# Performance work log

Hardware: AMD Instinct MI355X
Metric: run time of the kernel (lower is better)

## Reference

```python
import jax, jax.numpy as jnp
import numpy as np

B, T, D, H = 4, 2048, 1024, 16
HD = D // H  # 64


def setup_inputs() -> dict:
    key = jax.random.key(0)
    ks = jax.random.split(key, 5)
    return {
        "x": jax.random.normal(ks[0], (B, T, D), dtype=jnp.float32),
        "W_qkv": jax.random.normal(ks[1], (D, 3 * D), dtype=jnp.float32) * 0.02,
        "b_qkv": jax.random.normal(ks[2], (3 * D,), dtype=jnp.float32) * 0.02,
        "W_out": jax.random.normal(ks[3], (D, D), dtype=jnp.float32) * 0.02,
        "b_out": jax.random.normal(ks[4], (D,), dtype=jnp.float32) * 0.02,
        "mask": 1,
    }


def reference(x, W_qkv, b_qkv, W_out, b_out, mask):
    # fused QKV projection: (B,T,3D)
    qkv = x @ W_qkv + b_qkv
    # torch layout: view (B,T,H,3*hd) then chunk last dim into q,k,v
    qkv = qkv.reshape(B, T, H, 3, HD)
    q = qkv[..., 0, :].transpose(0, 2, 1, 3)  # (B,H,T,hd)
    k = qkv[..., 1, :].transpose(0, 2, 1, 3)
    v = qkv[..., 2, :].transpose(0, 2, 1, 3)
    scores = jnp.einsum('bhqd,bhkd->bhqk', q, k) / jnp.sqrt(jnp.float32(HD))
    if mask:
        causal = jnp.triu(jnp.ones((T, T), dtype=bool), k=1)
        scores = jnp.where(causal[None, None], jnp.float32(-jnp.inf), scores)
    attn = jax.nn.softmax(scores, axis=-1)
    out = jnp.einsum('bhqk,bhkd->bhqd', attn, v)  # (B,H,T,hd)
    out = out.transpose(0, 2, 1, 3).reshape(B, T, D)
    return out @ W_out + b_out
```

## Files before the change

### kernel.cpp

```cpp
#include <hip/hip_runtime.h>

typedef unsigned short u16;
typedef __bf16 bf16x8 __attribute__((ext_vector_type(8)));
typedef float f32x4 __attribute__((ext_vector_type(4)));
typedef float f32x16 __attribute__((ext_vector_type(16)));

#define DEV __device__ __forceinline__

constexpr int Bb = 4, Tt = 2048, Dd = 1024, Hh = 16, HDd = 64;
constexpr int MM = Bb * Tt;
constexpr float QSCALE = 0.125f * 1.4426950408889634f;

DEV u16 f2bf(float f) {
  unsigned u = __float_as_uint(f);
  u += 0x7fffu + ((u >> 16) & 1u);
  return (u16)(u >> 16);
}

DEV unsigned cvtpk(float a, float b) {
  unsigned r;
  asm("v_cvt_pk_bf16_f32 %0, %1, %2" : "=v"(r) : "v"(a), "v"(b));
  return r;
}

DEV void pswap(unsigned& a, unsigned& b) {
  asm("v_permlane32_swap_b32 %0, %1" : "+v"(a), "+v"(b));
}

DEV void gload_lds16(const u16* g, u16* l) {
  __builtin_amdgcn_global_load_lds(
      (const __attribute__((address_space(1))) void*)g,
      (__attribute__((address_space(3))) void*)l, 16, 0, 0);
}

__global__ __launch_bounds__(256) void cast_x_kernel(const float* __restrict__ in,
                                                     u16* __restrict__ out, int n8) {
  int i = blockIdx.x * 256 + threadIdx.x;
  if (i >= n8) return;
  const float4* p = (const float4*)in + (size_t)i * 2;
  float4 v0 = p[0], v1 = p[1];
  union { u16 u[8]; uint4 v; } t;
  t.u[0] = f2bf(v0.x); t.u[1] = f2bf(v0.y); t.u[2] = f2bf(v0.z); t.u[3] = f2bf(v0.w);
  t.u[4] = f2bf(v1.x); t.u[5] = f2bf(v1.y); t.u[6] = f2bf(v1.z); t.u[7] = f2bf(v1.w);
  ((uint4*)out)[i] = t.v;
}

__global__ __launch_bounds__(256) void wcast_t_kernel(const float* __restrict__ in,
                                                      u16* __restrict__ out, int K, int N) {
  __shared__ float tile[32][33];
  int n0 = blockIdx.x * 32, k0 = blockIdx.y * 32;
  int tx = threadIdx.x & 31, ty = threadIdx.x >> 5;
  #pragma unroll
  for (int yy = ty; yy < 32; yy += 8)
    tile[yy][tx] = in[(size_t)(k0 + yy) * N + n0 + tx];
  __syncthreads();
  #pragma unroll
  for (int yy = ty; yy < 32; yy += 8)
    out[(size_t)(n0 + yy) * K + k0 + tx] = f2bf(tile[tx][yy]);
}

DEV void stageA128(const u16* __restrict__ src, int row0, int k0, int ld, u16* lds) {
  int t = threadIdx.x;
  int r = t >> 2, slot = t & 3;
  int c = (slot ^ ((r >> 1) & 3)) << 3;
  gload_lds16(src + (size_t)(row0 + r) * ld + k0 + c, lds + (size_t)(t & ~63) * 8);
}
DEV void stageB256(const u16* __restrict__ src, int row0, int k0, int ld, u16* lds) {
  int t = threadIdx.x;
  #pragma unroll
  for (int j = 0; j < 2; ++j) {
    int e = j * 512 + t;
    int r = e >> 2, slot = e & 3;
    int c = (slot ^ ((r >> 1) & 3)) << 3;
    gload_lds16(src + (size_t)(row0 + r) * ld + k0 + c,
                lds + (size_t)(j * 512 + (t & ~63)) * 8);
  }
}

__global__ __launch_bounds__(512, 4) void gemm_qkv_kernel(
    const u16* __restrict__ A, const u16* __restrict__ Bt,
    const float* __restrict__ bias,
    u16* __restrict__ Qb, u16* __restrict__ Kb, u16* __restrict__ Vtb,
    int M, int N, int Kd) {
  __shared__ __align__(16) u16 SH[36864];
  int nx = N >> 8;
  int bid = blockIdx.y * nx + blockIdx.x;
  int nwg = (M >> 7) * nx;
  int swz = (bid & 7) * (nwg >> 3) + (bid >> 3);
  int m0 = (swz / nx) * 128, n0 = (swz % nx) * 256;

  int tid = threadIdx.x, l = tid & 63, w = tid >> 6;
  int lo = l & 15, g = l >> 4;
  int wm = (w >> 2) * 64, wn = (w & 3) * 64;
  f32x4 acc[4][4] = {};
  int nk = Kd >> 5;
  stageA128(A, m0, 0, Kd, SH);
  stageB256(Bt, n0, 0, Kd, SH + 12288);
  stageA128(A, m0, 32, Kd, SH + 4096);
  stageB256(Bt, n0, 32, Kd, SH + 12288 + 8192);
  asm volatile("s_waitcnt vmcnt(3)" ::: "memory");
  __builtin_amdgcn_s_barrier();
  for (int kt = 0; kt < nk; ++kt) {
    if (kt + 2 < nk) {
      int bi = (kt + 2) % 3;
      stageA128(A, m0, (kt + 2) * 32, Kd, SH + bi * 4096);
      stageB256(Bt, n0, (kt + 2) * 32, Kd, SH + 12288 + bi * 8192);
    }
    const u16* Ac = SH + (kt % 3) * 4096;
    const u16* Bc = SH + 12288 + (kt % 3) * 8192;
    bf16x8 a[4], b[4];
    #pragma unroll
    for (int i = 0; i < 4; ++i) {
      int row = wm + i * 16 + lo;
      a[i] = *(const bf16x8*)&Ac[row * 32 + ((g ^ ((row >> 1) & 3)) << 3)];
    }
    #pragma unroll
    for (int j = 0; j < 4; ++j) {
      int row = wn + j * 16 + lo;
      b[j] = *(const bf16x8*)&Bc[row * 32 + ((g ^ ((row >> 1) & 3)) << 3)];
    }
    __builtin_amdgcn_s_setprio(1);
    #pragma unroll
    for (int i = 0; i < 4; ++i)
      #pragma unroll
      for (int j = 0; j < 4; ++j)
        acc[i][j] = __builtin_amdgcn_mfma_f32_16x16x32_bf16(a[i], b[j], acc[i][j], 0, 0, 0);
    __builtin_amdgcn_s_setprio(0);
    if (kt + 2 < nk) {
      asm volatile("s_waitcnt vmcnt(3)" ::: "memory");
    } else {
      asm volatile("s_waitcnt vmcnt(0)" ::: "memory");
    }
    __builtin_amdgcn_s_barrier();
  }
  #pragma unroll
  for (int round = 0; round < 2; ++round) {
    if ((w >> 2) == round) {
      u16* ep = SH + (w & 3) * 4096;
      int nblk = n0 + wn;
      int hh = nblk / 192, which = (nblk % 192) >> 6;
      int mblk = m0 + wm;
      int b_ = mblk >> 11, t0 = mblk & (Tt - 1);
      if (which == 2) {
        #pragma unroll
        for (int j = 0; j < 4; ++j) {
          float bv = bias[nblk + j * 16 + lo];
          int rowp = j * 16 + lo;
          #pragma unroll
          for (int i = 0; i < 4; ++i) {
            int slotp = i * 2 + (g >> 1);
            #pragma unroll
            for (int r = 0; r < 4; ++r) {
              ep[rowp * 64 + ((slotp ^ (rowp & 7)) << 3) + (g & 1) * 4 + r] =
                  f2bf(acc[i][j][r] + bv);
            }
          }
        }
        asm volatile("s_waitcnt lgkmcnt(0)" ::: "memory");
        u16* dst = Vtb + (size_t)(b_ * Hh + hh) * HDd * Tt + t0;
        #pragma unroll
        for (int s = 0; s < 8; ++s) {
          int row = s * 8 + (l >> 3);
          int phys = ((l & 7) ^ (row & 7)) << 3;
          uint4 v = *(const uint4*)&ep[row * 64 + phys];
          *(uint4*)(dst + (size_t)row * Tt + (l & 7) * 8) = v;
        }
      } else {
        float qs = (which == 0) ? QSCALE : 1.0f;
        #pragma unroll
        for (int j = 0; j < 4; ++j) {
          float bv = bias[nblk + j * 16 + lo];
          int slot = j * 2 + (lo >> 3);
          #pragma unroll
          for (int i = 0; i < 4; ++i) {
            #pragma unroll
            for (int r = 0; r < 4; ++r) {
              int lrow = i * 16 + g * 4 + r;
              ep[lrow * 64 + ((slot ^ (lrow & 7)) << 3) + (lo & 7)] =
                  f2bf((acc[i][j][r] + bv) * qs);
            }
          }
        }
        asm volatile("s_waitcnt lgkmcnt(0)" ::: "memory");
        u16* dst = (which == 0) ? Qb : Kb;
        dst += ((size_t)(b_ * Hh + hh) * Tt + t0) * HDd;
        #pragma unroll
        for (int s = 0; s < 8; ++s) {
          int row = s * 8 + (l >> 3);
          int phys = ((l & 7) ^ (row & 7)) << 3;
          uint4 v = *(const uint4*)&ep[row * 64 + phys];
          *(uint4*)(dst + row * 64 + (l & 7) * 8) = v;
        }
      }
    }
    __syncthreads();
  }
}

__global__ __launch_bounds__(512, 4) void gemm_out256_kernel(
    const u16* __restrict__ A, const u16* __restrict__ Bt,
    const float* __restrict__ bias, float* __restrict__ Cf,
    int M, int N, int Kd) {
  __shared__ __align__(16) u16 SH[36864];
  int nx = N >> 8;
  int bid = blockIdx.y * nx + blockIdx.x;
  int nwg = (M >> 7) * nx;
  int swz = (bid & 7) * (nwg >> 3) + (bid >> 3);
  int m0 = (swz / nx) * 128, n0 = (swz % nx) * 256;

  int tid = threadIdx.x, l = tid & 63, w = tid >> 6;
  int lo = l & 15, g = l >> 4;
  int wm = (w >> 2) * 64, wn = (w & 3) * 64;
  f32x4 acc[4][4] = {};
  int nk = Kd >> 5;
  stageA128(A, m0, 0, Kd, SH);
  stageB256(Bt, n0, 0, Kd, SH + 12288);
  stageA128(A, m0, 32, Kd, SH + 4096);
  stageB256(Bt, n0, 32, Kd, SH + 12288 + 8192);
  asm volatile("s_waitcnt vmcnt(3)" ::: "memory");
  __builtin_amdgcn_s_barrier();
  for (int kt = 0; kt < nk; ++kt) {
    if (kt + 2 < nk) {
      int bi = (kt + 2) % 3;
      stageA128(A, m0, (kt + 2) * 32, Kd, SH + bi * 4096);
      stageB256(Bt, n0, (kt + 2) * 32, Kd, SH + 12288 + bi * 8192);
    }
    const u16* Ac = SH + (kt % 3) * 4096;
    const u16* Bc = SH + 12288 + (kt % 3) * 8192;
    bf16x8 a[4], b[4];
    #pragma unroll
    for (int i = 0; i < 4; ++i) {
      int row = wm + i * 16 + lo;
      a[i] = *(const bf16x8*)&Ac[row * 32 + ((g ^ ((row >> 1) & 3)) << 3)];
    }
    #pragma unroll
    for (int j = 0; j < 4; ++j) {
      int row = wn + j * 16 + lo;
      b[j] = *(const bf16x8*)&Bc[row * 32 + ((g ^ ((row >> 1) & 3)) << 3)];
    }
    __builtin_amdgcn_s_setprio(1);
    #pragma unroll
    for (int i = 0; i < 4; ++i)
      #pragma unroll
      for (int j = 0; j < 4; ++j)
        acc[i][j] = __builtin_amdgcn_mfma_f32_16x16x32_bf16(a[i], b[j], acc[i][j], 0, 0, 0);
    __builtin_amdgcn_s_setprio(0);
    if (kt + 2 < nk) {
      asm volatile("s_waitcnt vmcnt(3)" ::: "memory");
    } else {
      asm volatile("s_waitcnt vmcnt(0)" ::: "memory");
    }
    __builtin_amdgcn_s_barrier();
  }
  #pragma unroll
  for (int j = 0; j < 4; ++j) {
    int n = n0 + wn + j * 16 + lo;
    float bv = bias[n];
    #pragma unroll
    for (int i = 0; i < 4; ++i) {
      #pragma unroll
      for (int r = 0; r < 4; ++r) {
        int m = m0 + wm + i * 16 + g * 4 + r;
        Cf[(size_t)m * N + n] = acc[i][j][r] + bv;
      }
    }
  }
}

DEV void stage512(const u16* __restrict__ g, size_t rstride, u16* lds) {
  int t = threadIdx.x;
  int r = t >> 3, pp = t & 7;
  int lg = pp ^ (r & 7);
  gload_lds16(g + (size_t)r * rstride + lg * 8, lds + (size_t)(t & ~63) * 8);
}

DEV void build_pfrags(const f32x16& s, bf16x8& f0, bf16x8& f1) {
  unsigned w0 = cvtpk(s[0], s[1]),  w1 = cvtpk(s[2], s[3]);
  unsigned w2 = cvtpk(s[4], s[5]),  w3 = cvtpk(s[6], s[7]);
  unsigned w4 = cvtpk(s[8], s[9]),  w5 = cvtpk(s[10], s[11]);
  unsigned w6 = cvtpk(s[12], s[13]), w7 = cvtpk(s[14], s[15]);
  pswap(w0, w2);
  pswap(w1, w3);
  pswap(w4, w6);
  pswap(w5, w7);
  union { unsigned u[4]; bf16x8 v; } t0, t1;
  t0.u[0] = w0; t0.u[1] = w1; t0.u[2] = w2; t0.u[3] = w3;
  t1.u[0] = w4; t1.u[1] = w5; t1.u[2] = w6; t1.u[3] = w7;
  f0 = t0.v; f1 = t1.v;
}

DEV void write_o(u16* __restrict__ O, size_t rowbase, const f32x16& o0,
                 const f32x16& o1, float L, int hf) {
  float inv = 1.0f / L;
  #pragma unroll
  for (int m = 0; m < 4; ++m) {
    uint2 v0, v1;
    v0.x = cvtpk(o0[4 * m] * inv,     o0[4 * m + 1] * inv);
    v0.y = cvtpk(o0[4 * m + 2] * inv, o0[4 * m + 3] * inv);
    *(uint2*)(O + rowbase + m * 8 + hf * 4) = v0;
    v1.x = cvtpk(o1[4 * m] * inv,     o1[4 * m + 1] * inv);
    v1.y = cvtpk(o1[4 * m + 2] * inv, o1[4 * m + 3] * inv);
    *(uint2*)(O + rowbase + 32 + m * 8 + hf * 4) = v1;
  }
}

__global__ __launch_bounds__(512) void attn_kernel(const u16* __restrict__ Q,
                                                   const u16* __restrict__ K,
                                                   const u16* __restrict__ Vt,
                                                   u16* __restrict__ O) {
  __shared__ __align__(16) u16 Ks[4][4096];
  __shared__ __align__(16) u16 Vs[4][4096];
  __shared__ float MLs[8][64][2];
  __shared__ float OSs[4][64][4];
  int p = blockIdx.y & 7;
  int bh = ((int)blockIdx.y >> 3) * 8 + (int)blockIdx.x;
  int b_ = bh >> 4, h = bh & 15;
  const u16* Qp = Q + (size_t)bh * Tt * HDd;
  const u16* Kp = K + (size_t)bh * Tt * HDd;
  const u16* Vp = Vt + (size_t)bh * HDd * Tt;
  int tid = threadIdx.x, w = tid >> 6, l = tid & 63;
  int wq = w & 3, grp = w >> 2;
  int lq = l & 31, hf = l >> 5;
  int JA = 15 - p, JB = p;
  int ntA = 2 * JA + 2;
  constexpr int ntT = 34;

  int q0 = 128 * JA + 32 * wq;
  int qrow = q0 + lq;
  int swz = lq & 7;

  bf16x8 aq[4];
  #pragma unroll
  for (int s = 0; s < 4; ++s)
    aq[s] = *(const bf16x8*)(Qp + (size_t)qrow * HDd + s * 16 + hf * 8);

  f32x16 o0 = {}, o1 = {};
  float M = -1e30f, L = 0.f;

  stage512(Kp, HDd, Ks[0]);
  stage512(Vp, Tt, Vs[0]);
  stage512(Kp + (size_t)64 * HDd, HDd, Ks[1]);
  stage512(Vp + 64, Tt, Vs[1]);
  asm volatile("s_waitcnt vmcnt(0)" ::: "memory");
  __builtin_amdgcn_s_barrier();

  int jB = ntA >> 1;
  for (int j = 0; j < ntT / 2; ++j) {
    int t2 = 2 * j + 2;
    if (t2 < ntT) {
      int kt2 = (t2 < ntA ? t2 : t2 - ntA) * 64;
      stage512(Kp + (size_t)kt2 * HDd, HDd, Ks[t2 & 3]);
      stage512(Vp + kt2, Tt, Vs[t2 & 3]);
      int t3 = t2 + 1;
      int kt3 = (t3 < ntA ? t3 : t3 - ntA) * 64;
      stage512(Kp + (size_t)kt3 * HDd, HDd, Ks[t3 & 3]);
      stage512(Vp + kt3, Tt, Vs[t3 & 3]);
    }
    if (j == jB) {
      MLs[w][l][0] = M; MLs[w][l][1] = L;
      asm volatile("s_waitcnt lgkmcnt(0)" ::: "memory");
      __builtin_amdgcn_s_barrier();
      float Mb = MLs[w ^ 4][l][0], Lb = MLs[w ^ 4][l][1];
      float Mstar = fmaxf(M, Mb);
      float ss = __builtin_amdgcn_exp2f(M - Mstar);
      float sb = __builtin_amdgcn_exp2f(Mb - Mstar);
      float Lm = L * ss + Lb * sb;
      #pragma unroll
      for (int r = 0; r < 16; ++r) { o0[r] *= ss; o1[r] *= ss; }
      #pragma unroll
      for (int c = 0; c < 8; ++c) {
        if (w >= 4) {
          #pragma unroll
          for (int k = 0; k < 4; ++k)
            OSs[wq][l][k] = (c < 4) ? o0[c * 4 + k] : o1[(c - 4) * 4 + k];
        }
        asm volatile("s_waitcnt lgkmcnt(0)" ::: "memory");
        __builtin_amdgcn_s_barrier();
        if (w < 4) {
          #pragma unroll
          for (int k = 0; k < 4; ++k) {
            float v = OSs[wq][l][k];
            if (c < 4) o0[c * 4 + k] += v; else o1[(c - 4) * 4 + k] += v;
          }
        }
        asm volatile("s_waitcnt lgkmcnt(0)" ::: "memory");
        __builtin_amdgcn_s_barrier();
      }
      if (w < 4) {
        size_t rbA = ((size_t)b_ * Tt + qrow) * Dd + h * HDd;
        write_o(O, rbA, o0, o1, Lm, hf);
      }
      #pragma unroll
      for (int r = 0; r < 16; ++r) { o0[r] = 0.f; o1[r] = 0.f; }
      M = -1e30f; L = 0.f;
      q0 = 128 * JB + 32 * wq;
      qrow = q0 + lq;
      #pragma unroll
      for (int s = 0; s < 4; ++s)
        aq[s] = *(const bf16x8*)(Qp + (size_t)qrow * HDd + s * 16 + hf * 8);
    }
    int myt = 2 * j + grp;
    int kt = (myt < ntA ? myt : myt - ntA) * 64;
    const u16* Kc = Ks[myt & 3];
    const u16* Vc = Vs[myt & 3];
    if (kt < q0 + 32) {
      f32x16 s0 = {}, s1 = {};
      __builtin_amdgcn_s_setprio(1);
      #pragma unroll
      for (int ds = 0; ds < 4; ++ds) {
        int slot = 2 * ds + hf;
        bf16x8 k0 = *(const bf16x8*)&Kc[lq * 64 + ((slot ^ swz) << 3)];
        bf16x8 k1 = *(const bf16x8*)&Kc[(32 + lq) * 64 + ((slot ^ swz) << 3)];
        s0 = __builtin_amdgcn_mfma_f32_32x32x16_bf16(k0, aq[ds], s0, 0, 0, 0);
        s1 = __builtin_amdgcn_mfma_f32_32x32x16_bf16(k1, aq[ds], s1, 0, 0, 0);
      }
      __builtin_amdgcn_s_setprio(0);
      if (kt + 63 > q0) {
        #pragma unroll
        for (int r = 0; r < 16; ++r) {
          int kg = kt + (r & 3) + 8 * (r >> 2) + 4 * hf;
          if (kg > qrow)      s0[r] = -INFINITY;
          if (kg + 32 > qrow) s1[r] = -INFINITY;
        }
      }
      float mx_[16];
      #pragma unroll
      for (int r = 0; r < 16; ++r) mx_[r] = fmaxf(s0[r], s1[r]);
      #pragma unroll
      for (int st = 8; st >= 1; st >>= 1)
        #pragma unroll
        for (int r = 0; r < 16; ++r) if (r < st) mx_[r] = fmaxf(mx_[r], mx_[r + st]);
      float mx = fmaxf(mx_[0], __shfl_xor(mx_[0], 32));
      float sc = 1.f;
      if (!__all(mx <= M + 8.f)) {
        float Mn = fmaxf(M, mx);
        sc = __builtin_amdgcn_exp2f(M - Mn);
        M = Mn;
        #pragma unroll
        for (int r = 0; r < 16; ++r) { o0[r] *= sc; o1[r] *= sc; }
      }
      #pragma unroll
      for (int r = 0; r < 16; ++r) {
        s0[r] = __builtin_amdgcn_exp2f(s0[r] - M);
        s1[r] = __builtin_amdgcn_exp2f(s1[r] - M);
      }
      float ls_[16];
      #pragma unroll
      for (int r = 0; r < 16; ++r) ls_[r] = s0[r] + s1[r];
      #pragma unroll
      for (int st = 8; st >= 1; st >>= 1)
        #pragma unroll
        for (int r = 0; r < 16; ++r) if (r < st) ls_[r] += ls_[r + st];
      float ls = ls_[0] + __shfl_xor(ls_[0], 32);
      L = L * sc + ls;
      bf16x8 pf0, pf1, pf2, pf3;
      build_pfrags(s0, pf0, pf1);
      build_pfrags(s1, pf2, pf3);
      __builtin_amdgcn_s_setprio(1);
      #pragma unroll
      for (int ks = 0; ks < 4; ++ks) {
        int slot = 2 * ks + hf;
        bf16x8 v0 = *(const bf16x8*)&Vc[lq * 64 + ((slot ^ swz) << 3)];
        bf16x8 v1 = *(const bf16x8*)&Vc[(32 + lq) * 64 + ((slot ^ swz) << 3)];
        bf16x8 pf = (ks == 0) ? pf0 : (ks == 1) ? pf1 : (ks == 2) ? pf2 : pf3;
        o0 = __builtin_amdgcn_mfma_f32_32x32x16_bf16(v0, pf, o0, 0, 0, 0);
        o1 = __builtin_amdgcn_mfma_f32_32x32x16_bf16(v1, pf, o1, 0, 0, 0);
      }
      __builtin_amdgcn_s_setprio(0);
    }
    asm volatile("s_waitcnt vmcnt(0)" ::: "memory");
    __builtin_amdgcn_s_barrier();
  }

  MLs[w][l][0] = M; MLs[w][l][1] = L;
  asm volatile("s_waitcnt lgkmcnt(0)" ::: "memory");
  __builtin_amdgcn_s_barrier();
  float Mb = MLs[w ^ 4][l][0], Lb = MLs[w ^ 4][l][1];
  float Mstar = fmaxf(M, Mb);
  float ss = __builtin_amdgcn_exp2f(M - Mstar);
  float sb = __builtin_amdgcn_exp2f(Mb - Mstar);
  float Lm = L * ss + Lb * sb;
  #pragma unroll
  for (int r = 0; r < 16; ++r) { o0[r] *= ss; o1[r] *= ss; }
  #pragma unroll
  for (int c = 0; c < 8; ++c) {
    if (w >= 4) {
      #pragma unroll
      for (int k = 0; k < 4; ++k)
        OSs[wq][l][k] = (c < 4) ? o0[c * 4 + k] : o1[(c - 4) * 4 + k];
    }
    asm volatile("s_waitcnt lgkmcnt(0)" ::: "memory");
    __builtin_amdgcn_s_barrier();
    if (w < 4) {
      #pragma unroll
      for (int k = 0; k < 4; ++k) {
        float v = OSs[wq][l][k];
        if (c < 4) o0[c * 4 + k] += v; else o1[(c - 4) * 4 + k] += v;
      }
    }
    asm volatile("s_waitcnt lgkmcnt(0)" ::: "memory");
    __builtin_amdgcn_s_barrier();
  }
  if (w < 4) {
    size_t rbB = ((size_t)b_ * Tt + qrow) * Dd + h * HDd;
    write_o(O, rbB, o0, o1, Lm, hf);
  }
}

extern "C" void kernel_launch(void* const* d_in, const int* in_sizes, int n_in,
                              void* d_out, int out_size, void* d_ws, size_t ws_size,
                              hipStream_t stream) {
  const float* x    = (const float*)d_in[0];
  const float* Wqkv = (const float*)d_in[1];
  const float* bqkv = (const float*)d_in[2];
  const float* Wout = (const float*)d_in[3];
  const float* bout = (const float*)d_in[4];
  float* out = (float*)d_out;
  char* ws = (char*)d_ws;

  u16* xb    = (u16*)(ws + 0);
  u16* Ob    = (u16*)(ws + 0);
  u16* Wqkvt = (u16*)(ws + 16777216);
  u16* Woutt = (u16*)(ws + 23068672);
  u16* Qb    = (u16*)(ws + 25165824);
  u16* Kb    = (u16*)(ws + 41943040);
  u16* Vtb   = (u16*)(ws + 58720256);

  cast_x_kernel<<<4096, 256, 0, stream>>>(x, xb, (MM * Dd) / 8);
  wcast_t_kernel<<<dim3(96, 32), 256, 0, stream>>>(Wqkv, Wqkvt, Dd, 3 * Dd);
  wcast_t_kernel<<<dim3(32, 32), 256, 0, stream>>>(Wout, Woutt, Dd, Dd);
  gemm_qkv_kernel<<<dim3(12, 64), 512, 0, stream>>>(
      xb, Wqkvt, bqkv, Qb, Kb, Vtb, MM, 3 * Dd, Dd);
  attn_kernel<<<dim3(8, 64), 512, 0, stream>>>(Qb, Kb, Vtb, Ob);
  gemm_out256_kernel<<<dim3(4, 64), 512, 0, stream>>>(
      Ob, Woutt, bout, out, MM, Dd, Dd);
}
```

Baseline: 174.6 us.

## Split attention KV loop across four wave groups with 1024-thread blocks

Doubles the attention block to 16 waves, so four wave groups each take a different KV tile per iteration instead of two. The KV ring grows to 8 LDS slots and four tiles are staged per step. Partial softmax states are combined with a two-level merge (xor 8, then xor 4). The aim is more parallelism per query tile and half as many loop iterations. In exchange it pads the A-phase tile count to a multiple of four, which may add masked or wasted tiles, and adds LDS pressure, more barrier rounds in the merge, and launch_bounds(1024,1) register limits.

```diff
diff --git a/kernel.cpp b/kernel.cpp
--- a/kernel.cpp
+++ b/kernel.cpp
@@ -267,13 +267,6 @@
   }
 }
 
-DEV void stage512(const u16* __restrict__ g, size_t rstride, u16* lds) {
-  int t = threadIdx.x;
-  int r = t >> 3, pp = t & 7;
-  int lg = pp ^ (r & 7);
-  gload_lds16(g + (size_t)r * rstride + lg * 8, lds + (size_t)(t & ~63) * 8);
-}
-
 DEV void build_pfrags(const f32x16& s, bf16x8& f0, bf16x8& f1) {
   unsigned w0 = cvtpk(s[0], s[1]),  w1 = cvtpk(s[2], s[3]);
   unsigned w2 = cvtpk(s[4], s[5]),  w3 = cvtpk(s[6], s[7]);
@@ -304,14 +297,14 @@
   }
 }
 
-__global__ __launch_bounds__(512) void attn_kernel(const u16* __restrict__ Q,
-                                                   const u16* __restrict__ K,
-                                                   const u16* __restrict__ Vt,
-                                                   u16* __restrict__ O) {
-  __shared__ __align__(16) u16 Ks[4][4096];
-  __shared__ __align__(16) u16 Vs[4][4096];
-  __shared__ float MLs[8][64][2];
-  __shared__ float OSs[4][64][4];
+__global__ __launch_bounds__(1024, 1) void attn_kernel(const u16* __restrict__ Q,
+                                                       const u16* __restrict__ K,
+                                                       const u16* __restrict__ Vt,
+                                                       u16* __restrict__ O) {
+  __shared__ __align__(16) u16 Ks[8][4096];
+  __shared__ __align__(16) u16 Vs[8][4096];
+  __shared__ float MLs[16][64][2];
+  __shared__ float OSs[8][64][4];
   int p = blockIdx.y & 7;
   int bh = ((int)blockIdx.y >> 3) * 8 + (int)blockIdx.x;
   int b_ = bh >> 4, h = bh & 15;
@@ -323,7 +316,8 @@
   int lq = l & 31, hf = l >> 5;
   int JA = 15 - p, JB = p;
   int ntA = 2 * JA + 2;
-  constexpr int ntT = 34;
+  int ntAp = (ntA + 3) & ~3;
+  int jA = ntAp >> 2;
 
   int q0 = 128 * JA + 32 * wq;
   int qrow = q0 + lq;
@@ -337,58 +331,71 @@
   f32x16 o0 = {}, o1 = {};
   float M = -1e30f, L = 0.f;
 
-  stage512(Kp, HDd, Ks[0]);
-  stage512(Vp, Tt, Vs[0]);
-  stage512(Kp + (size_t)64 * HDd, HDd, Ks[1]);
-  stage512(Vp + 64, Tt, Vs[1]);
+  auto slot_kt = [&](int s) { return (s < ntAp ? s : s - ntAp) * 64; };
+  auto stage2K = [&](int s) {
+    int s2 = s + (tid >> 9), c = tid & 511;
+    int kt2 = slot_kt(s2);
+    int r = c >> 3, pp = c & 7;
+    int lg = pp ^ (r & 7);
+    gload_lds16(Kp + (size_t)(kt2 + r) * HDd + lg * 8,
+                Ks[s2 & 7] + (size_t)(c & ~63) * 8);
+  };
+  auto stage2V = [&](int s) {
+    int s2 = s + (tid >> 9), c = tid & 511;
+    int kt2 = slot_kt(s2);
+    int r = c >> 3, pp = c & 7;
+    int lg = pp ^ (r & 7);
+    gload_lds16(Vp + kt2 + (size_t)r * Tt + lg * 8,
+                Vs[s2 & 7] + (size_t)(c & ~63) * 8);
+  };
+  auto merge_stage = [&](int bit) {
+    MLs[w][l][0] = M; MLs[w][l][1] = L;
+    asm volatile("s_waitcnt lgkmcnt(0)" ::: "memory");
+    __builtin_amdgcn_s_barrier();
+    float Mb = MLs[w ^ bit][l][0], Lb = MLs[w ^ bit][l][1];
+    float Mstar = fmaxf(M, Mb);
+    float ssc = __builtin_amdgcn_exp2f(M - Mstar);
+    float sbc = __builtin_amdgcn_exp2f(Mb - Mstar);
+    #pragma unroll
+    for (int r = 0; r < 16; ++r) { o0[r] *= ssc; o1[r] *= ssc; }
+    L = L * ssc + Lb * sbc;
+    M = Mstar;
+    bool sender   = (bit == 8) ? (w >= 8) : (w >= 4 && w < 8);
+    bool receiver = (bit == 8) ? (w < 8)  : (w < 4);
+    #pragma unroll
+    for (int c = 0; c < 8; ++c) {
+      if (sender) {
+        #pragma unroll
+        for (int k = 0; k < 4; ++k)
+          OSs[w ^ bit][l][k] = (c < 4) ? o0[c * 4 + k] : o1[(c - 4) * 4 + k];
+      }
+      asm volatile("s_waitcnt lgkmcnt(0)" ::: "memory");
+      __builtin_amdgcn_s_barrier();
+      if (receiver) {
+        #pragma unroll
+        for (int k = 0; k < 4; ++k) {
+          float v = OSs[w][l][k];
+          if (c < 4) o0[c * 4 + k] += v; else o1[(c - 4) * 4 + k] += v;
+        }
+      }
+      asm volatile("s_waitcnt lgkmcnt(0)" ::: "memory");
+      __builtin_amdgcn_s_barrier();
+    }
+  };
+
+  stage2K(0); stage2K(2); stage2V(0); stage2V(2);
   asm volatile("s_waitcnt vmcnt(0)" ::: "memory");
   __builtin_amdgcn_s_barrier();
 
-  int jB = ntA >> 1;
-  for (int j = 0; j < ntT / 2; ++j) {
-    int t2 = 2 * j + 2;
-    if (t2 < ntT) {
-      int kt2 = (t2 < ntA ? t2 : t2 - ntA) * 64;
-      stage512(Kp + (size_t)kt2 * HDd, HDd, Ks[t2 & 3]);
-      stage512(Vp + kt2, Tt, Vs[t2 & 3]);
-      int t3 = t2 + 1;
-      int kt3 = (t3 < ntA ? t3 : t3 - ntA) * 64;
-      stage512(Kp + (size_t)kt3 * HDd, HDd, Ks[t3 & 3]);
-      stage512(Vp + kt3, Tt, Vs[t3 & 3]);
-    }
-    if (j == jB) {
-      MLs[w][l][0] = M; MLs[w][l][1] = L;
-      asm volatile("s_waitcnt lgkmcnt(0)" ::: "memory");
-      __builtin_amdgcn_s_barrier();
-      float Mb = MLs[w ^ 4][l][0], Lb = MLs[w ^ 4][l][1];
-      float Mstar = fmaxf(M, Mb);
-      float ss = __builtin_amdgcn_exp2f(M - Mstar);
-      float sb = __builtin_amdgcn_exp2f(Mb - Mstar);
-      float Lm = L * ss + Lb * sb;
-      #pragma unroll
-      for (int r = 0; r < 16; ++r) { o0[r] *= ss; o1[r] *= ss; }
-      #pragma unroll
-      for (int c = 0; c < 8; ++c) {
-        if (w >= 4) {
-          #pragma unroll
-          for (int k = 0; k < 4; ++k)
-            OSs[wq][l][k] = (c < 4) ? o0[c * 4 + k] : o1[(c - 4) * 4 + k];
-        }
-        asm volatile("s_waitcnt lgkmcnt(0)" ::: "memory");
-        __builtin_amdgcn_s_barrier();
-        if (w < 4) {
-          #pragma unroll
-          for (int k = 0; k < 4; ++k) {
-            float v = OSs[wq][l][k];
-            if (c < 4) o0[c * 4 + k] += v; else o1[(c - 4) * 4 + k] += v;
-          }
-        }
-        asm volatile("s_waitcnt lgkmcnt(0)" ::: "memory");
-        __builtin_amdgcn_s_barrier();
-      }
+  for (int j = 0; j < 9; ++j) {
+    int snext = 4 * (j + 1);
+    if (snext < 36) { stage2K(snext); stage2K(snext + 2); stage2V(snext); stage2V(snext + 2); }
+    if (j == jA) {
+      merge_stage(8);
+      merge_stage(4);
       if (w < 4) {
         size_t rbA = ((size_t)b_ * Tt + qrow) * Dd + h * HDd;
-        write_o(O, rbA, o0, o1, Lm, hf);
+        write_o(O, rbA, o0, o1, L, hf);
       }
       #pragma unroll
       for (int r = 0; r < 16; ++r) { o0[r] = 0.f; o1[r] = 0.f; }
@@ -399,18 +406,18 @@
       for (int s = 0; s < 4; ++s)
         aq[s] = *(const bf16x8*)(Qp + (size_t)qrow * HDd + s * 16 + hf * 8);
     }
-    int myt = 2 * j + grp;
-    int kt = (myt < ntA ? myt : myt - ntA) * 64;
-    const u16* Kc = Ks[myt & 3];
-    const u16* Vc = Vs[myt & 3];
+    int slot = 4 * j + grp;
+    int kt = (j < jA ? slot : slot - ntAp) * 64;
+    const u16* Kc = Ks[slot & 7];
+    const u16* Vc = Vs[slot & 7];
     if (kt < q0 + 32) {
       f32x16 s0 = {}, s1 = {};
       __builtin_amdgcn_s_setprio(1);
       #pragma unroll
       for (int ds = 0; ds < 4; ++ds) {
-        int slot = 2 * ds + hf;
-        bf16x8 k0 = *(const bf16x8*)&Kc[lq * 64 + ((slot ^ swz) << 3)];
-        bf16x8 k1 = *(const bf16x8*)&Kc[(32 + lq) * 64 + ((slot ^ swz) << 3)];
+        int slt = 2 * ds + hf;
+        bf16x8 k0 = *(const bf16x8*)&Kc[lq * 64 + ((slt ^ swz) << 3)];
+        bf16x8 k1 = *(const bf16x8*)&Kc[(32 + lq) * 64 + ((slt ^ swz) << 3)];
         s0 = __builtin_amdgcn_mfma_f32_32x32x16_bf16(k0, aq[ds], s0, 0, 0, 0);
         s1 = __builtin_amdgcn_mfma_f32_32x32x16_bf16(k1, aq[ds], s1, 0, 0, 0);
       }
@@ -459,9 +466,9 @@
       __builtin_amdgcn_s_setprio(1);
       #pragma unroll
       for (int ks = 0; ks < 4; ++ks) {
-        int slot = 2 * ks + hf;
-        bf16x8 v0 = *(const bf16x8*)&Vc[lq * 64 + ((slot ^ swz) << 3)];
-        bf16x8 v1 = *(const bf16x8*)&Vc[(32 + lq) * 64 + ((slot ^ swz) << 3)];
+        int slt = 2 * ks + hf;
+        bf16x8 v0 = *(const bf16x8*)&Vc[lq * 64 + ((slt ^ swz) << 3)];
+        bf16x8 v1 = *(const bf16x8*)&Vc[(32 + lq) * 64 + ((slt ^ swz) << 3)];
         bf16x8 pf = (ks == 0) ? pf0 : (ks == 1) ? pf1 : (ks == 2) ? pf2 : pf3;
         o0 = __builtin_amdgcn_mfma_f32_32x32x16_bf16(v0, pf, o0, 0, 0, 0);
         o1 = __builtin_amdgcn_mfma_f32_32x32x16_bf16(v1, pf, o1, 0, 0, 0);
@@ -472,38 +479,11 @@
     __builtin_amdgcn_s_barrier();
   }
 
-  MLs[w][l][0] = M; MLs[w][l][1] = L;
-  asm volatile("s_waitcnt lgkmcnt(0)" ::: "memory");
-  __builtin_amdgcn_s_barrier();
-  float Mb = MLs[w ^ 4][l][0], Lb = MLs[w ^ 4][l][1];
-  float Mstar = fmaxf(M, Mb);
-  float ss = __builtin_amdgcn_exp2f(M - Mstar);
-  float sb = __builtin_amdgcn_exp2f(Mb - Mstar);
-  float Lm = L * ss + Lb * sb;
-  #pragma unroll
-  for (int r = 0; r < 16; ++r) { o0[r] *= ss; o1[r] *= ss; }
-  #pragma unroll
-  for (int c = 0; c < 8; ++c) {
-    if (w >= 4) {
-      #pragma unroll
-      for (int k = 0; k < 4; ++k)
-        OSs[wq][l][k] = (c < 4) ? o0[c * 4 + k] : o1[(c - 4) * 4 + k];
-    }
-    asm volatile("s_waitcnt lgkmcnt(0)" ::: "memory");
-    __builtin_amdgcn_s_barrier();
-    if (w < 4) {
-      #pragma unroll
-      for (int k = 0; k < 4; ++k) {
-        float v = OSs[wq][l][k];
-        if (c < 4) o0[c * 4 + k] += v; else o1[(c - 4) * 4 + k] += v;
-      }
-    }
-    asm volatile("s_waitcnt lgkmcnt(0)" ::: "memory");
-    __builtin_amdgcn_s_barrier();
-  }
+  merge_stage(8);
+  merge_stage(4);
   if (w < 4) {
     size_t rbB = ((size_t)b_ * Tt + qrow) * Dd + h * HDd;
-    write_o(O, rbB, o0, o1, Lm, hf);
+    write_o(O, rbB, o0, o1, L, hf);
   }
 }
 
@@ -531,7 +511,7 @@
   wcast_t_kernel<<<dim3(32, 32), 256, 0, stream>>>(Wout, Woutt, Dd, Dd);
   gemm_qkv_kernel<<<dim3(12, 64), 512, 0, stream>>>(
       xb, Wqkvt, bqkv, Qb, Kb, Vtb, MM, 3 * Dd, Dd);
-  attn_kernel<<<dim3(8, 64), 512, 0, stream>>>(Qb, Kb, Vtb, Ob);
+  attn_kernel<<<dim3(8, 64), 1024, 0, stream>>>(Qb, Kb, Vtb, Ob);
   gemm_out256_kernel<<<dim3(4, 64), 512, 0, stream>>>(
       Ob, Woutt, bout, out, MM, Dd, Dd);
 }
```

Result: slower. 180.1 us (+3.2%).
